# Performance work log

Measured on AMD Instinct MI355X. Metric: run time of the kernel, lower is better.

## Reference

```python
import jax, jax.numpy as jnp
import numpy as np

DIM = 768
HEADS = 12
HEAD_DIM = DIM // HEADS
SCALE = DIM ** (-0.5)  # NOTE: module scales by full dim, not head_dim


def setup_inputs() -> dict:
    key = jax.random.key(0)
    k1, k2, k3 = jax.random.split(key, 3)
    B, N = 4, 2048
    x = jax.random.normal(k1, (B, N, DIM), dtype=jnp.float32)
    W_qkv = jax.random.normal(k2, (DIM, 3 * DIM), dtype=jnp.float32) * (DIM ** -0.5)
    W_proj = jax.random.normal(k3, (DIM, DIM), dtype=jnp.float32) * (DIM ** -0.5)
    b_proj = jnp.zeros((DIM,), dtype=jnp.float32)
    return {"x": x, "W_qkv": W_qkv, "W_proj": W_proj, "b_proj": b_proj}


def reference(x, W_qkv, W_proj, b_proj):
    B, N, C = x.shape
    qkv = x @ W_qkv  # [B, N, 3C]
    qkv = qkv.reshape(B, N, 3, HEADS, HEAD_DIM)
    qkv = jnp.transpose(qkv, (2, 0, 3, 1, 4))  # [3, B, H, N, hd]
    q, k, v = qkv[0], qkv[1], qkv[2]
    att = jnp.einsum('bhnd,bhmd->bhnm', q, k) * SCALE
    att = jax.nn.softmax(att, axis=-1)
    # drop=0.0 -> dropout is identity
    out = jnp.einsum('bhnm,bhmd->bhnd', att, v)  # [B, H, N, hd]
    out = jnp.transpose(out, (0, 2, 1, 3)).reshape(B, N, C)
    return out @ W_proj + b_proj
```

## Files before the change

kernel.cpp:

```cpp
#include <hip/hip_runtime.h>
#include <hip/hip_bf16.h>

#define HEADS 12
#define HD    64
#define SEQ   2048
#define CDIM  768
#define QKV_SCALE 0.03608439182435161f
#define LOG2E 1.4426950408889634f
#define SM_C (QKV_SCALE * LOG2E)

typedef __attribute__((ext_vector_type(8))) short bf16x8;
typedef __attribute__((ext_vector_type(4))) float f32x4;
typedef __attribute__((ext_vector_type(4))) unsigned short usx4;
typedef __attribute__((ext_vector_type(8))) unsigned short usx8;
typedef __attribute__((ext_vector_type(2))) unsigned int uix2;
typedef __attribute__((ext_vector_type(4))) unsigned int uix4;

__device__ __forceinline__ unsigned short f2bf(float f) {
  union { __hip_bfloat16 h; unsigned short u; } c;
  c.h = __float2bfloat16(f);
  return c.u;
}

__device__ __forceinline__ float exp2_fast(float x) {
  float r; asm("v_exp_f32 %0, %1" : "=v"(r) : "v"(x)); return r;
}

__device__ __forceinline__ unsigned int cvt_pk_bf16(float lo, float hi) {
  unsigned int r; asm("v_cvt_pk_bf16_f32 %0, %1, %2" : "=v"(r) : "v"(lo), "v"(hi)); return r;
}

__device__ __forceinline__ void gload_lds16(const unsigned short* g, unsigned short* l) {
  __builtin_amdgcn_global_load_lds(
      (__attribute__((address_space(1))) void*)(g),
      (__attribute__((address_space(3))) void*)(l), 16, 0, 0);
}

__global__ __launch_bounds__(256) void k_prep(
    const float* __restrict__ x, unsigned short* __restrict__ xb,
    const float* __restrict__ Wqkv, unsigned short* __restrict__ WqkvT,
    const float* __restrict__ Wproj, unsigned short* __restrict__ WprojT) {
  __shared__ float tile[32][33];
  const int b = blockIdx.x;
  if (b < 3072) {
    int i = b * 256 + threadIdx.x;
    const float4* s4 = (const float4*)x;
    float4 a = s4[i * 2 + 0];
    float4 d = s4[i * 2 + 1];
    usx8 r;
    r[0] = f2bf(a.x); r[1] = f2bf(a.y); r[2] = f2bf(a.z); r[3] = f2bf(a.w);
    r[4] = f2bf(d.x); r[5] = f2bf(d.y); r[6] = f2bf(d.z); r[7] = f2bf(d.w);
    *(usx8*)&xb[i * 8] = r;
    return;
  }
  const float* src; unsigned short* dst; int C, c0, k0;
  if (b < 4800) {
    int tb = b - 3072;
    src = Wqkv; dst = WqkvT; C = 2304;
    c0 = (tb % 72) * 32; k0 = (tb / 72) * 32;
  } else {
    int tb = b - 4800;
    src = Wproj; dst = WprojT; C = 768;
    c0 = (tb % 24) * 32; k0 = (tb / 24) * 32;
  }
  int tx = threadIdx.x & 31;
  int ty = threadIdx.x >> 5;
#pragma unroll
  for (int i = 0; i < 32; i += 8)
    tile[ty + i][tx] = src[(size_t)(k0 + ty + i) * C + c0 + tx];
  __syncthreads();
#pragma unroll
  for (int i = 0; i < 32; i += 8)
    dst[(size_t)(c0 + ty + i) * 768 + k0 + tx] = f2bf(tile[tx][ty + i]);
}

__global__ __launch_bounds__(256) void k_qkv_gemm(
    const unsigned short* __restrict__ A,
    const unsigned short* __restrict__ Bt,
    unsigned short* __restrict__ Qb, unsigned short* __restrict__ Kb,
    unsigned short* __restrict__ Vt) {
  __shared__ unsigned short As[2][128 * 64];
  __shared__ unsigned short Bs[2][128 * 64];
  const int lane = threadIdx.x & 63, w = threadIdx.x >> 6;
  const int wm = w >> 1, wn = w & 1;
  const int id = blockIdx.y * 18 + blockIdx.x;
  const int lin = (id & 7) * 144 + (id >> 3);
  const int r0 = (lin / 18) * 128, c0 = (lin % 18) * 128;
  f32x4 acc[4][4] = {};

  const unsigned short* aptr[4];
  const unsigned short* bptr[4];
#pragma unroll
  for (int iss = 0; iss < 4; ++iss) {
    int e = (w * 4 + iss) * 512 + lane * 8;
    int row = e >> 6, cc = ((e >> 3) & 7) ^ (row & 7);
    aptr[iss] = A  + (size_t)(r0 + row) * 768 + cc * 8;
    bptr[iss] = Bt + (size_t)(c0 + row) * 768 + cc * 8;
  }

  auto STAGE = [&](int k0, int b) {
#pragma unroll
    for (int iss = 0; iss < 4; ++iss) {
      gload_lds16(aptr[iss] + k0, &As[b][(w * 4 + iss) * 512]);
      gload_lds16(bptr[iss] + k0, &Bs[b][(w * 4 + iss) * 512]);
    }
  };

  STAGE(0, 0);
  asm volatile("s_waitcnt vmcnt(0)" ::: "memory");
  __syncthreads();

  auto KSTEP = [&](int t, int buf) {
    if (t + 1 < 12) STAGE((t + 1) * 64, buf ^ 1);
#pragma unroll
    for (int ks = 0; ks < 2; ++ks) {
      bf16x8 af[4], bfr[4];
#pragma unroll
      for (int f = 0; f < 4; ++f) {
        int ar = wm * 64 + f * 16 + (lane & 15);
        int ac = (ks * 4 + (lane >> 4)) ^ (ar & 7);
        af[f] = *(const bf16x8*)&As[buf][ar * 64 + ac * 8];
        int br = wn * 64 + f * 16 + (lane & 15);
        int bc = (ks * 4 + (lane >> 4)) ^ (br & 7);
        bfr[f] = *(const bf16x8*)&Bs[buf][br * 64 + bc * 8];
      }
#pragma unroll
      for (int fm = 0; fm < 4; ++fm)
#pragma unroll
        for (int fn = 0; fn < 4; ++fn)
          acc[fm][fn] = __builtin_amdgcn_mfma_f32_16x16x32_bf16(af[fm], bfr[fn], acc[fm][fn], 0, 0, 0);
    }
    asm volatile("s_waitcnt vmcnt(0)" ::: "memory");
    __syncthreads();
  };

  for (int t = 0; t < 12; t += 2) {
    KSTEP(t, 0);
    KSTEP(t + 1, 1);
  }

  const int which = c0 / 768;
  const float qsc = (which == 0) ? SM_C : 1.0f;
#pragma unroll
  for (int fm = 0; fm < 4; ++fm) {
    int gr0 = r0 + wm * 64 + fm * 16 + ((lane >> 4) << 2);
    int bb = gr0 >> 11, n0 = gr0 & 2047;
#pragma unroll
    for (int fn = 0; fn < 4; ++fn) {
      int gc = c0 + wn * 64 + fn * 16 + (lane & 15);
      int rem = gc - which * 768;
      int h = rem >> 6, d = rem & 63;
      int bh = bb * HEADS + h;
      f32x4 v = acc[fm][fn];
      if (which == 2) {
        usx4 p;
        p[0] = f2bf(v[0]); p[1] = f2bf(v[1]); p[2] = f2bf(v[2]); p[3] = f2bf(v[3]);
        *(usx4*)&Vt[(size_t)(bh * 64 + d) * 2048 + n0] = p;
      } else {
        unsigned short* dst = (which == 0 ? Qb : Kb) + (size_t)(bh * 2048 + n0) * 64 + d;
        dst[0]   = f2bf(v[0] * qsc);
        dst[64]  = f2bf(v[1] * qsc);
        dst[128] = f2bf(v[2] * qsc);
        dst[192] = f2bf(v[3] * qsc);
      }
    }
  }
}

__global__ __launch_bounds__(256, 2) void k_attn(
    const unsigned short* __restrict__ Qb, const unsigned short* __restrict__ Kb,
    const unsigned short* __restrict__ Vt, unsigned short* __restrict__ Ob) {
  __shared__ unsigned short Ksm[2][64 * 64];
  __shared__ unsigned short Vsm[2][64 * 64];
  const int lane = threadIdx.x & 63, w = threadIdx.x >> 6;
  const int g = lane >> 4, c = lane & 15;

  int id = blockIdx.x + (blockIdx.y << 4);
  int lin = (id & 7) * 96 + (id >> 3);
  int bx = lin & 15, bh = lin >> 4;
  const int q0 = bx * 128 + w * 32;
  const int bb = bh / HEADS, h = bh % HEADS;

  const unsigned short* Qp = Qb + (size_t)bh * SEQ * HD;
  const unsigned short* Kp = Kb + (size_t)bh * SEQ * HD;
  const unsigned short* Vp = Vt + (size_t)bh * HD * SEQ;

  bf16x8 aQ[2][2];
#pragma unroll
  for (int qf = 0; qf < 2; ++qf)
#pragma unroll
    for (int ks = 0; ks < 2; ++ks)
      aQ[qf][ks] = *(const bf16x8*)&Qp[(size_t)(q0 + qf * 16 + c) * 64 + ks * 32 + g * 8];

  float lrun[2] = {0.f, 0.f};
  f32x4 accOT[4][2] = {};
  const f32x4 fzero = {0.f, 0.f, 0.f, 0.f};

  int offf[2][4];
#pragma unroll
  for (int ks = 0; ks < 2; ++ks)
#pragma unroll
    for (int f = 0; f < 4; ++f) {
      int row = f * 16 + c;
      offf[ks][f] = row * 64 + (((ks * 4 + g) ^ (row & 7)) * 8);
    }

  const int eo0 = (w * 2 + 0) * 512 + lane * 8;
  const int row0 = eo0 >> 6, cc0 = ((eo0 >> 3) & 7) ^ (row0 & 7);
  const int eo1 = (w * 2 + 1) * 512 + lane * 8;
  const int row1 = eo1 >> 6, cc1 = ((eo1 >> 3) & 7) ^ (row1 & 7);
  const unsigned short* kga = Kp + (size_t)row0 * 64 + cc0 * 8;
  const unsigned short* kgb = Kp + (size_t)row1 * 64 + cc1 * 8;
  const unsigned short* vga = Vp + (size_t)row0 * 2048 + cc0 * 8;
  const unsigned short* vgb = Vp + (size_t)row1 * 2048 + cc1 * 8;

  gload_lds16(kga, &Ksm[0][(w * 2 + 0) * 512]);
  gload_lds16(kgb, &Ksm[0][(w * 2 + 1) * 512]);
  gload_lds16(vga, &Vsm[0][(w * 2 + 0) * 512]);
  gload_lds16(vgb, &Vsm[0][(w * 2 + 1) * 512]);
  asm volatile("s_waitcnt vmcnt(0)" ::: "memory");
  __syncthreads();

  auto TILE = [&](int t, int buf) {
    if (t + 1 < 32) {
      gload_lds16(kga + (t + 1) * 4096, &Ksm[buf ^ 1][(w * 2 + 0) * 512]);
      gload_lds16(kgb + (t + 1) * 4096, &Ksm[buf ^ 1][(w * 2 + 1) * 512]);
      gload_lds16(vga + (t + 1) * 64,   &Vsm[buf ^ 1][(w * 2 + 0) * 512]);
      gload_lds16(vgb + (t + 1) * 64,   &Vsm[buf ^ 1][(w * 2 + 1) * 512]);
    }

    bf16x8 kf0[4], kf1[4];
#pragma unroll
    for (int fm = 0; fm < 4; ++fm) {
      kf0[fm] = *(const bf16x8*)&Ksm[buf][offf[0][fm]];
      kf1[fm] = *(const bf16x8*)&Ksm[buf][offf[1][fm]];
    }
    f32x4 st[4][2];
    __builtin_amdgcn_s_setprio(1);
#pragma unroll
    for (int fm = 0; fm < 4; ++fm)
#pragma unroll
      for (int qf = 0; qf < 2; ++qf)
        st[fm][qf] = __builtin_amdgcn_mfma_f32_16x16x32_bf16(kf0[fm], aQ[qf][0], fzero, 0, 0, 0);
#pragma unroll
    for (int fm = 0; fm < 4; ++fm)
#pragma unroll
      for (int qf = 0; qf < 2; ++qf)
        st[fm][qf] = __builtin_amdgcn_mfma_f32_16x16x32_bf16(kf1[fm], aQ[qf][1], st[fm][qf], 0, 0, 0);
    __builtin_amdgcn_s_setprio(0);

    uix4 pfrag[2][2];
#pragma unroll
    for (int qf = 0; qf < 2; ++qf) {
      float p[4][4];
      float ts[4];
#pragma unroll
      for (int fm = 0; fm < 4; ++fm) {
        p[fm][0] = exp2_fast(st[fm][qf][0]);
        p[fm][1] = exp2_fast(st[fm][qf][1]);
        p[fm][2] = exp2_fast(st[fm][qf][2]);
        p[fm][3] = exp2_fast(st[fm][qf][3]);
        ts[fm] = (p[fm][0] + p[fm][1]) + (p[fm][2] + p[fm][3]);
      }
      lrun[qf] += (ts[0] + ts[1]) + (ts[2] + ts[3]);

#pragma unroll
      for (int ks = 0; ks < 2; ++ks)
#pragma unroll
        for (int tt = 0; tt < 2; ++tt) {
          unsigned int a = cvt_pk_bf16(p[2 * ks][2 * tt], p[2 * ks][2 * tt + 1]);
          unsigned int b = cvt_pk_bf16(p[2 * ks + 1][2 * tt], p[2 * ks + 1][2 * tt + 1]);
          uix2 s1 = __builtin_amdgcn_permlane32_swap(a, b, false, false);
          uix2 s2 = __builtin_amdgcn_permlane16_swap(s1[0], s1[1], false, false);
          pfrag[ks][qf][tt] = s2[0];
          pfrag[ks][qf][2 + tt] = s2[1];
        }
    }

    bf16x8 vf0[4], vf1[4];
#pragma unroll
    for (int fd = 0; fd < 4; ++fd) {
      vf0[fd] = *(const bf16x8*)&Vsm[buf][offf[0][fd]];
      vf1[fd] = *(const bf16x8*)&Vsm[buf][offf[1][fd]];
    }
    __builtin_amdgcn_s_setprio(1);
#pragma unroll
    for (int fd = 0; fd < 4; ++fd)
#pragma unroll
      for (int qf = 0; qf < 2; ++qf) {
        accOT[fd][qf] = __builtin_amdgcn_mfma_f32_16x16x32_bf16(
            vf0[fd], *(const bf16x8*)&pfrag[0][qf], accOT[fd][qf], 0, 0, 0);
        accOT[fd][qf] = __builtin_amdgcn_mfma_f32_16x16x32_bf16(
            vf1[fd], *(const bf16x8*)&pfrag[1][qf], accOT[fd][qf], 0, 0, 0);
      }
    __builtin_amdgcn_s_setprio(0);

    asm volatile("s_waitcnt vmcnt(0)" ::: "memory");
    __syncthreads();
  };

  for (int kt = 0; kt < 32; kt += 2) {
    TILE(kt, 0);
    TILE(kt + 1, 1);
  }

#pragma unroll
  for (int qf = 0; qf < 2; ++qf) {
    float l = lrun[qf];
    l += __shfl_xor(l, 16);
    l += __shfl_xor(l, 32);
    float rl = 1.0f / l;
    int n = q0 + qf * 16 + c;
#pragma unroll
    for (int fd = 0; fd < 4; ++fd) {
      f32x4 v = accOT[fd][qf];
      usx4 pk;
      pk[0] = f2bf(v[0] * rl); pk[1] = f2bf(v[1] * rl);
      pk[2] = f2bf(v[2] * rl); pk[3] = f2bf(v[3] * rl);
      *(usx4*)&Ob[(size_t)(bb * SEQ + n) * CDIM + h * HD + fd * 16 + 4 * g] = pk;
    }
  }
}

__global__ __launch_bounds__(256) void k_proj_gemm(
    const unsigned short* __restrict__ A,
    const unsigned short* __restrict__ Bt,
    const float* __restrict__ bias, float* __restrict__ out) {
  __shared__ unsigned short As[2][64 * 64];
  __shared__ unsigned short Bs[2][128 * 64];
  const int lane = threadIdx.x & 63, w = threadIdx.x >> 6;
  const int wm = w & 1, wn = w >> 1;
  const int id = blockIdx.y * 6 + blockIdx.x;
  const int lin = (id & 7) * 96 + (id >> 3);
  const int r0 = (lin / 6) * 64, c0 = (lin % 6) * 128;
  f32x4 acc[2][4] = {};

  const unsigned short* aptr[2];
  const unsigned short* bptr[4];
#pragma unroll
  for (int iss = 0; iss < 2; ++iss) {
    int e = (w * 2 + iss) * 512 + lane * 8;
    int row = e >> 6, cc = ((e >> 3) & 7) ^ (row & 7);
    aptr[iss] = A + (size_t)(r0 + row) * 768 + cc * 8;
  }
#pragma unroll
  for (int iss = 0; iss < 4; ++iss) {
    int e = (w * 4 + iss) * 512 + lane * 8;
    int row = e >> 6, cc = ((e >> 3) & 7) ^ (row & 7);
    bptr[iss] = Bt + (size_t)(c0 + row) * 768 + cc * 8;
  }

  auto STAGE = [&](int k0, int b) {
#pragma unroll
    for (int iss = 0; iss < 2; ++iss)
      gload_lds16(aptr[iss] + k0, &As[b][(w * 2 + iss) * 512]);
#pragma unroll
    for (int iss = 0; iss < 4; ++iss)
      gload_lds16(bptr[iss] + k0, &Bs[b][(w * 4 + iss) * 512]);
  };

  STAGE(0, 0);
  asm volatile("s_waitcnt vmcnt(0)" ::: "memory");
  __syncthreads();

  auto KSTEP = [&](int t, int buf) {
    if (t + 1 < 12) STAGE((t + 1) * 64, buf ^ 1);
#pragma unroll
    for (int ks = 0; ks < 2; ++ks) {
      bf16x8 af[2], bfr[4];
#pragma unroll
      for (int f = 0; f < 2; ++f) {
        int ar = wm * 32 + f * 16 + (lane & 15);
        int ac = (ks * 4 + (lane >> 4)) ^ (ar & 7);
        af[f] = *(const bf16x8*)&As[buf][ar * 64 + ac * 8];
      }
#pragma unroll
      for (int f = 0; f < 4; ++f) {
        int br = wn * 64 + f * 16 + (lane & 15);
        int bc = (ks * 4 + (lane >> 4)) ^ (br & 7);
        bfr[f] = *(const bf16x8*)&Bs[buf][br * 64 + bc * 8];
      }
#pragma unroll
      for (int fm = 0; fm < 2; ++fm)
#pragma unroll
        for (int fn = 0; fn < 4; ++fn)
          acc[fm][fn] = __builtin_amdgcn_mfma_f32_16x16x32_bf16(af[fm], bfr[fn], acc[fm][fn], 0, 0, 0);
    }
    asm volatile("s_waitcnt vmcnt(0)" ::: "memory");
    __syncthreads();
  };

  for (int t = 0; t < 12; t += 2) {
    KSTEP(t, 0);
    KSTEP(t + 1, 1);
  }

#pragma unroll
  for (int fm = 0; fm < 2; ++fm) {
    int gr0 = r0 + wm * 32 + fm * 16 + ((lane >> 4) << 2);
#pragma unroll
    for (int fn = 0; fn < 4; ++fn) {
      int gc = c0 + wn * 64 + fn * 16 + (lane & 15);
      float bsv = bias[gc];
      f32x4 v = acc[fm][fn];
#pragma unroll
      for (int r = 0; r < 4; ++r)
        out[(size_t)(gr0 + r) * CDIM + gc] = v[r] + bsv;
    }
  }
}

extern "C" void kernel_launch(void* const* d_in, const int* in_sizes, int n_in,
                              void* d_out, int out_size, void* d_ws, size_t ws_size,
                              hipStream_t stream) {
  const float* x      = (const float*)d_in[0];
  const float* W_qkv  = (const float*)d_in[1];
  const float* W_proj = (const float*)d_in[2];
  const float* b_proj = (const float*)d_in[3];
  float* out = (float*)d_out;

  unsigned short* ws     = (unsigned short*)d_ws;
  unsigned short* xb     = ws;
  unsigned short* WqkvT  = xb + 6291456;
  unsigned short* WprojT = WqkvT + 1769472;
  unsigned short* Qb     = WprojT + 589824;
  unsigned short* Kb     = Qb + 6291456;
  unsigned short* Vt     = Kb + 6291456;
  unsigned short* Ob     = Vt + 6291456;

  k_prep<<<5376, 256, 0, stream>>>(x, xb, W_qkv, WqkvT, W_proj, WprojT);
  k_qkv_gemm<<<dim3(18, 64), 256, 0, stream>>>(xb, WqkvT, Qb, Kb, Vt);
  k_attn<<<dim3(16, 48), 256, 0, stream>>>(Qb, Kb, Vt, Ob);
  k_proj_gemm<<<dim3(6, 128), 256, 0, stream>>>(Ob, WprojT, b_proj, out);
}
```

Before: 137.2 us.

## Shrink QKV GEMM K-tile to 32 with new swizzle and MFMA priority

```diff
diff --git a/kernel.cpp b/kernel.cpp
--- a/kernel.cpp
+++ b/kernel.cpp
@@ -79,30 +79,40 @@
     const unsigned short* __restrict__ Bt,
     unsigned short* __restrict__ Qb, unsigned short* __restrict__ Kb,
     unsigned short* __restrict__ Vt) {
-  __shared__ unsigned short As[2][128 * 64];
-  __shared__ unsigned short Bs[2][128 * 64];
+  __shared__ unsigned short As[2][128 * 32];
+  __shared__ unsigned short Bs[2][128 * 32];
   const int lane = threadIdx.x & 63, w = threadIdx.x >> 6;
+  const int g = lane >> 4, c = lane & 15;
   const int wm = w >> 1, wn = w & 1;
   const int id = blockIdx.y * 18 + blockIdx.x;
   const int lin = (id & 7) * 144 + (id >> 3);
   const int r0 = (lin / 18) * 128, c0 = (lin % 18) * 128;
   f32x4 acc[4][4] = {};
 
-  const unsigned short* aptr[4];
-  const unsigned short* bptr[4];
-#pragma unroll
-  for (int iss = 0; iss < 4; ++iss) {
-    int e = (w * 4 + iss) * 512 + lane * 8;
-    int row = e >> 6, cc = ((e >> 3) & 7) ^ (row & 7);
-    aptr[iss] = A  + (size_t)(r0 + row) * 768 + cc * 8;
-    bptr[iss] = Bt + (size_t)(c0 + row) * 768 + cc * 8;
+  const unsigned short* aptr[2];
+  const unsigned short* bptr[2];
+#pragma unroll
+  for (int i = 0; i < 2; ++i) {
+    int e = (w * 2 + i) * 512 + lane * 8;
+    int row = e >> 5;
+    int cc = ((e >> 3) & 3) ^ ((row >> 1) & 3);
+    aptr[i] = A  + (size_t)(r0 + row) * 768 + cc * 8;
+    bptr[i] = Bt + (size_t)(c0 + row) * 768 + cc * 8;
+  }
+
+  const int sg = g ^ ((c >> 1) & 3);
+  int offA[4], offB[4];
+#pragma unroll
+  for (int f = 0; f < 4; ++f) {
+    offA[f] = (wm * 64 + f * 16 + c) * 32 + sg * 8;
+    offB[f] = (wn * 64 + f * 16 + c) * 32 + sg * 8;
   }
 
   auto STAGE = [&](int k0, int b) {
 #pragma unroll
-    for (int iss = 0; iss < 4; ++iss) {
-      gload_lds16(aptr[iss] + k0, &As[b][(w * 4 + iss) * 512]);
-      gload_lds16(bptr[iss] + k0, &Bs[b][(w * 4 + iss) * 512]);
+    for (int i = 0; i < 2; ++i) {
+      gload_lds16(aptr[i] + k0, &As[b][(w * 2 + i) * 512]);
+      gload_lds16(bptr[i] + k0, &Bs[b][(w * 2 + i) * 512]);
     }
   };
 
@@ -111,30 +121,25 @@
   __syncthreads();
 
   auto KSTEP = [&](int t, int buf) {
-    if (t + 1 < 12) STAGE((t + 1) * 64, buf ^ 1);
-#pragma unroll
-    for (int ks = 0; ks < 2; ++ks) {
-      bf16x8 af[4], bfr[4];
-#pragma unroll
-      for (int f = 0; f < 4; ++f) {
-        int ar = wm * 64 + f * 16 + (lane & 15);
-        int ac = (ks * 4 + (lane >> 4)) ^ (ar & 7);
-        af[f] = *(const bf16x8*)&As[buf][ar * 64 + ac * 8];
-        int br = wn * 64 + f * 16 + (lane & 15);
-        int bc = (ks * 4 + (lane >> 4)) ^ (br & 7);
-        bfr[f] = *(const bf16x8*)&Bs[buf][br * 64 + bc * 8];
-      }
-#pragma unroll
-      for (int fm = 0; fm < 4; ++fm)
-#pragma unroll
-        for (int fn = 0; fn < 4; ++fn)
-          acc[fm][fn] = __builtin_amdgcn_mfma_f32_16x16x32_bf16(af[fm], bfr[fn], acc[fm][fn], 0, 0, 0);
-    }
+    if (t + 1 < 24) STAGE((t + 1) * 32, buf ^ 1);
+    bf16x8 af[4], bfr[4];
+#pragma unroll
+    for (int f = 0; f < 4; ++f) {
+      af[f]  = *(const bf16x8*)&As[buf][offA[f]];
+      bfr[f] = *(const bf16x8*)&Bs[buf][offB[f]];
+    }
+    __builtin_amdgcn_s_setprio(1);
+#pragma unroll
+    for (int fm = 0; fm < 4; ++fm)
+#pragma unroll
+      for (int fn = 0; fn < 4; ++fn)
+        acc[fm][fn] = __builtin_amdgcn_mfma_f32_16x16x32_bf16(af[fm], bfr[fn], acc[fm][fn], 0, 0, 0);
+    __builtin_amdgcn_s_setprio(0);
     asm volatile("s_waitcnt vmcnt(0)" ::: "memory");
     __syncthreads();
   };
 
-  for (int t = 0; t < 12; t += 2) {
+  for (int t = 0; t < 24; t += 2) {
     KSTEP(t, 0);
     KSTEP(t + 1, 1);
   }
```

After: 144.1 us. 1.05x slower.
